# Kernel tuning notes

Measured on AMD Instinct MI355X. Metric: run time of the kernel, lower is better.

The kernel has to match this reference:

```python
import jax, jax.numpy as jnp
import numpy as np

T, H, NH, HD, I = 2048, 2048, 16, 128, 8192
EPS = 1e-6


def rotate_every_two(x):
    # result[..., 2i] = -x[..., 2i+1]; result[..., 2i+1] = x[..., 2i]
    x1 = x[..., ::2]
    x2 = x[..., 1::2]
    return jnp.stack((-x2, x1), axis=-1).reshape(x.shape)


def setup_inputs() -> dict:
    key = jax.random.key(0)
    ks = jax.random.split(key, 10)
    x = jax.random.normal(ks[0], (T, H), dtype=jnp.float32)
    normed_ages = jax.random.normal(ks[1], (T,), dtype=jnp.float32)
    sin = jax.random.uniform(ks[2], (T, 1, HD), dtype=jnp.float32)
    cos = jax.random.uniform(ks[3], (T, 1, HD), dtype=jnp.float32)
    attn_bias = jax.random.normal(ks[4], (1, NH, T, T), dtype=jnp.float32) * 0.02
    norm_w = jnp.ones((H,), dtype=jnp.float32)
    w_in = jax.random.normal(ks[5], (H, 3 * H + 2 * I), dtype=jnp.float32) / np.sqrt(H)
    b_in = jnp.zeros((3 * H + 2 * I,), dtype=jnp.float32)
    w_out = jax.random.normal(ks[6], (H + I, H), dtype=jnp.float32) / np.sqrt(H + I)
    b_out = jnp.zeros((H,), dtype=jnp.float32)
    return {"x": x, "normed_ages": normed_ages, "sin": sin, "cos": cos,
            "attn_bias": attn_bias, "norm_w": norm_w, "w_in": w_in,
            "b_in": b_in, "w_out": w_out, "b_out": b_out}


def reference(x, normed_ages, sin, cos, attn_bias, norm_w, b_in, b_out, w_in, w_out):
    # RMSNorm
    xn = x * jax.lax.rsqrt(jnp.mean(x * x, axis=-1, keepdims=True) + EPS) * norm_w
    # use_normed_ages: overwrite last two feature columns
    xn = xn.at[:, -2].set(normed_ages)
    xn = xn.at[:, -1].set(normed_ages * normed_ages)
    # fused input projection: [T, 2I (ff) | 3H (qkv)]
    t = xn @ w_in + b_in
    ff = t[:, : 2 * I]
    qkv = t[:, 2 * I:].reshape(T, 3, NH, HD)
    q = qkv[:, 0] * cos + rotate_every_two(qkv[:, 0]) * sin  # [T, NH, HD]
    k = qkv[:, 1] * cos + rotate_every_two(qkv[:, 1]) * sin
    v = qkv[:, 2]
    # attention (xformers memory_efficient_attention semantics, scale 1/sqrt(HD))
    scores = jnp.einsum('thd,shd->hts', q, k) / np.sqrt(HD) + attn_bias[0]
    probs = jax.nn.softmax(scores, axis=-1)
    attn = jnp.einsum('hts,shd->thd', probs, v).reshape(T, H)
    # SwiGLU
    x1, x2 = ff[:, :I], ff[:, I:]
    ff = jax.nn.silu(x1) * x2
    combined = jnp.concatenate((attn, ff), axis=-1)  # [T, H+I]
    return combined @ w_out + b_out
```

## Files before the change

kernel.cpp:

```cpp
#include <hip/hip_runtime.h>
#include <stdint.h>

typedef unsigned short u16;
typedef __attribute__((ext_vector_type(8))) short short8;
typedef __attribute__((ext_vector_type(4))) short short4v;
typedef __attribute__((ext_vector_type(4))) float floatx4;

#define T_DIM 2048
#define NH    16
#define HD    128
#define H_DIM 2048
#define I_DIM 8192
#define NCOL1 22528
#define NCOL2 10240
#define PADW  1036
#define KSPLIT 4
#define KSLEN  (NCOL2 / KSPLIT)

__device__ __forceinline__ float bf2f(u16 b) {
  union { uint32_t u; float f; } x; x.u = ((uint32_t)b) << 16; return x.f;
}
__device__ __forceinline__ u16 f2bf(float f) {
  union { float f; uint32_t u; } x; x.f = f;
  uint32_t r = x.u + 0x7fffu + ((x.u >> 16) & 1u);
  return (u16)(r >> 16);
}

__device__ __forceinline__ void gl_lds16(const void* g, void* l) {
  __builtin_amdgcn_global_load_lds((const __attribute__((address_space(1))) void*)g,
                                   (__attribute__((address_space(3))) void*)l, 16, 0, 0);
}

__device__ __forceinline__ floatx4 mfma32(short8 a, short8 b, floatx4 c) {
  return __builtin_amdgcn_mfma_f32_16x16x32_bf16(a, b, c, 0, 0, 0);
}
__device__ __forceinline__ floatx4 mfma16(short4v a, short4v b, floatx4 c) {
#if __has_builtin(__builtin_amdgcn_mfma_f32_16x16x16bf16_1k)
  return __builtin_amdgcn_mfma_f32_16x16x16bf16_1k(a, b, c, 0, 0, 0);
#else
  asm volatile("v_mfma_f32_16x16x16_bf16 %0, %1, %2, %0" : "+v"(c) : "v"(a), "v"(b));
  return c;
#endif
}

__global__ __launch_bounds__(256) void rmsnorm_k(
    const float* __restrict__ x, const float* __restrict__ ages,
    const float* __restrict__ w, u16* __restrict__ xn) {
  int t = blockIdx.x, tid = threadIdx.x;
  const float* xr = x + (size_t)t * H_DIM;
  floatx4 a = *(const floatx4*)(xr + tid * 8);
  floatx4 b = *(const floatx4*)(xr + tid * 8 + 4);
  float ss = a[0]*a[0]+a[1]*a[1]+a[2]*a[2]+a[3]*a[3]
           + b[0]*b[0]+b[1]*b[1]+b[2]*b[2]+b[3]*b[3];
#pragma unroll
  for (int off = 32; off >= 1; off >>= 1) ss += __shfl_xor(ss, off);
  __shared__ float red[4];
  if ((tid & 63) == 0) red[tid >> 6] = ss;
  __syncthreads();
  float tot = red[0] + red[1] + red[2] + red[3];
  float rms = rsqrtf(tot * (1.0f / H_DIM) + 1e-6f);
  const float* wr = w + tid * 8;
  float v[8] = {a[0],a[1],a[2],a[3],b[0],b[1],b[2],b[3]};
  short8 o;
#pragma unroll
  for (int i = 0; i < 8; ++i) o[i] = (short)f2bf(v[i] * rms * wr[i]);
  if (tid == 255) {
    float ag = ages[t];
    o[6] = (short)f2bf(ag);
    o[7] = (short)f2bf(ag * ag);
  }
  *(short8*)(xn + (size_t)t * H_DIM + tid * 8) = o;
}

__global__ __launch_bounds__(256) void transpose_f32_bf16(
    const float* __restrict__ in, u16* __restrict__ out, int K, int N) {
  __shared__ float tile[32][33];
  int n0 = blockIdx.x * 32, k0 = blockIdx.y * 32;
  int c = threadIdx.x & 31, r = threadIdx.x >> 5;
#pragma unroll
  for (int i = 0; i < 4; ++i) {
    int kk = r + i * 8;
    tile[c][kk] = in[(size_t)(k0 + kk) * N + n0 + c];
  }
  __syncthreads();
#pragma unroll
  for (int i = 0; i < 4; ++i) {
    int nn = r + i * 8;
    out[(size_t)(n0 + nn) * K + k0 + c] = f2bf(tile[nn][c]);
  }
}

template<int OUTF>
__global__ __launch_bounds__(256, 2) void gemm_bt(
    const u16* __restrict__ A, const u16* __restrict__ B,
    const float* __restrict__ bias, void* __restrict__ Cout,
    int M, int N, int K, int klen) {
  __shared__ __align__(16) u16 sm[32768];
  int nbm = M >> 7, nbn = N >> 7;
  int per = nbm * nbn;
  int nwg = per * (K / klen);
  int bid = blockIdx.x;
  int swz = (bid & 7) * (nwg >> 3) + (bid >> 3);
  int sp = swz / per, rr = swz % per;
  int bn = rr / nbm, bm = rr % nbm;
  int kbeg = sp * klen;
  int tid = threadIdx.x, lane = tid & 63, w = tid >> 6;
  int wr = tid >> 7, wc = (tid >> 6) & 1;
  int lq = lane & 15, lg = lane >> 4;

  int srow = lane >> 2;
  int scol = (((lane & 3) ^ ((lane >> 3) & 3)) << 3);
  const u16* Ag0 = A + (size_t)(bm * 128 + w * 32 + srow) * K + kbeg + scol;
  const u16* Ag1 = Ag0 + (size_t)16 * K;
  const u16* Bg0 = B + (size_t)(bn * 128 + w * 32 + srow) * K + kbeg + scol;
  const u16* Bg1 = Bg0 + (size_t)16 * K;
  u16* Ad0 = sm + w * 1024 + lane * 8;
  u16* Ad1 = Ad0 + 512;
  u16* Bd0 = sm + 4096 + w * 1024 + lane * 8;
  u16* Bd1 = Bd0 + 512;

  int xorc = ((lq >> 1) & 3) << 3;
  int aoff = (wr * 64 + lq) * 32 + ((lg * 8) ^ xorc);
  int boff = 4096 + (wc * 64 + lq) * 32 + ((lg * 8) ^ xorc);

  floatx4 acc[4][4] = {};
  const int NT = klen >> 5;

  auto STAGE = [&](int t) {
    int sl = (t & 3) * 8192;
    int ko = t * 32;
    gl_lds16(Ag0 + ko, Ad0 + sl);
    gl_lds16(Ag1 + ko, Ad1 + sl);
    gl_lds16(Bg0 + ko, Bd0 + sl);
    gl_lds16(Bg1 + ko, Bd1 + sl);
  };

  STAGE(0); STAGE(1); STAGE(2);
  asm volatile("s_waitcnt vmcnt(8)\n\ts_barrier" ::: "memory");

  for (int t = 0; t < NT; ++t) {
    if (t + 3 < NT) STAGE(t + 3);
    const u16* sb = sm + (t & 3) * 8192;
    short8 af[4], bf[4];
#pragma unroll
    for (int i = 0; i < 4; ++i) af[i] = *(const short8*)(sb + aoff + i * 512);
#pragma unroll
    for (int i = 0; i < 4; ++i) bf[i] = *(const short8*)(sb + boff + i * 512);
    __builtin_amdgcn_s_setprio(1);
#pragma unroll
    for (int mi = 0; mi < 4; ++mi)
#pragma unroll
      for (int ni = 0; ni < 4; ++ni)
        acc[mi][ni] = mfma32(af[mi], bf[ni], acc[mi][ni]);
    __builtin_amdgcn_s_setprio(0);
    if (t + 3 < NT) asm volatile("s_waitcnt vmcnt(8)\n\ts_barrier" ::: "memory");
    else            asm volatile("s_waitcnt vmcnt(0)\n\ts_barrier" ::: "memory");
  }

#pragma unroll
  for (int mi = 0; mi < 4; ++mi) {
#pragma unroll
    for (int ni = 0; ni < 4; ++ni) {
      int col = bn * 128 + wc * 64 + ni * 16 + lq;
      float bv = (OUTF == 2) ? 0.f : bias[col];
#pragma unroll
      for (int j = 0; j < 4; ++j) {
        int row = bm * 128 + wr * 64 + mi * 16 + lg * 4 + j;
        float vv = acc[mi][ni][j] + bv;
        if (OUTF == 0)      ((u16*)Cout)[(size_t)row * N + col] = f2bf(vv);
        else if (OUTF == 1) ((float*)Cout)[(size_t)row * N + col] = vv;
        else ((float*)Cout)[(size_t)sp * M * N + (size_t)row * N + col] = vv;
      }
    }
  }
}

__global__ __launch_bounds__(256) void reduce_split(
    const float* __restrict__ part, const float* __restrict__ bias,
    float* __restrict__ out) {
  size_t idx = ((size_t)blockIdx.x * 256 + threadIdx.x) * 4;
  int col = (int)(idx & (H_DIM - 1));
  floatx4 acc = *(const floatx4*)(bias + col);
#pragma unroll
  for (int s = 0; s < KSPLIT; ++s) {
    floatx4 p = *(const floatx4*)(part + (size_t)s * T_DIM * H_DIM + idx);
#pragma unroll
    for (int j = 0; j < 4; ++j) acc[j] += p[j];
  }
  *(floatx4*)(out + idx) = acc;
}

__global__ __launch_bounds__(256) void rope_split(
    const u16* __restrict__ tb, const float* __restrict__ sinp, const float* __restrict__ cosp,
    u16* __restrict__ qb, u16* __restrict__ kf, u16* __restrict__ vf) {
  __shared__ u16 vtile[32][130];
  int t0 = blockIdx.x * 32, h = blockIdx.y, tid = threadIdx.x;
  int r = tid >> 3, d0 = (tid & 7) << 4;
  int t = t0 + r;
  const u16* base = tb + (size_t)t * NCOL1 + 2 * I_DIM + h * HD + d0;
  const float* cp = cosp + (size_t)t * HD + d0;
  const float* sp = sinp + (size_t)t * HD + d0;
  float cv[16], sv[16];
#pragma unroll
  for (int i = 0; i < 16; i += 4) {
    *(floatx4*)(cv + i) = *(const floatx4*)(cp + i);
    *(floatx4*)(sv + i) = *(const floatx4*)(sp + i);
  }
#pragma unroll
  for (int s = 0; s < 2; ++s) {
    const u16* src = base + s * (NH * HD);
    short8 x0 = *(const short8*)src;
    short8 x1 = *(const short8*)(src + 8);
    float xf[16];
#pragma unroll
    for (int i = 0; i < 8; ++i) { xf[i] = bf2f((u16)x0[i]); xf[8 + i] = bf2f((u16)x1[i]); }
    short8 o0, o1;
#pragma unroll
    for (int i = 0; i < 8; i += 2) {
      o0[i]     = (short)f2bf(xf[i] * cv[i] - xf[i + 1] * sv[i]);
      o0[i + 1] = (short)f2bf(xf[i + 1] * cv[i + 1] + xf[i] * sv[i + 1]);
      o1[i]     = (short)f2bf(xf[8 + i] * cv[8 + i] - xf[9 + i] * sv[8 + i]);
      o1[i + 1] = (short)f2bf(xf[9 + i] * cv[9 + i] + xf[8 + i] * sv[9 + i]);
    }
    if (s == 0) {
      u16* dst = qb + ((size_t)h * T_DIM + t) * HD + d0;
      *(short8*)dst = o0;
      *(short8*)(dst + 8) = o1;
    } else {
      int s16 = t >> 4, tt = d0 >> 5, lg0 = (d0 >> 3) & 3;
      size_t cb = (((size_t)h * 128 + s16) * 4 + tt) * 512 + ((t & 15) + 16 * lg0) * 8;
      *(short8*)(kf + cb) = o0;
      *(short8*)(kf + cb + 128) = o1;
    }
  }
  short8 v0 = *(const short8*)(base + 2 * NH * HD);
  short8 v1 = *(const short8*)(base + 2 * NH * HD + 8);
#pragma unroll
  for (int i = 0; i < 8; ++i) {
    vtile[r][d0 + i]     = (u16)v0[i];
    vtile[r][d0 + 8 + i] = (u16)v1[i];
  }
  __syncthreads();
  {
    int d = tid >> 1, th = (tid & 1) << 4;
    int s16 = (t0 + th) >> 4;
    int dp = d >> 5, par = (d >> 4) & 1, lqv = d & 15;
    size_t cb = (((size_t)h * 128 + s16) * 4 + dp) * 512 + par * 4;
#pragma unroll
    for (int lg = 0; lg < 4; ++lg) {
      short4v g;
#pragma unroll
      for (int j = 0; j < 4; ++j) g[j] = (short)vtile[th + lg * 4 + j][d];
      *(short4v*)(vf + cb + (size_t)(lqv + 16 * lg) * 8) = g;
    }
  }
}

__global__ __launch_bounds__(256) void silu_mul(
    const u16* __restrict__ tb, u16* __restrict__ comb) {
  int idx = blockIdx.x * 256 + threadIdx.x;
  int t = idx >> 10;
  int j = (idx & 1023) << 3;
  const u16* p1 = tb + (size_t)t * NCOL1 + j;
  const u16* p2 = p1 + I_DIM;
  short8 a = *(const short8*)p1;
  short8 b = *(const short8*)p2;
  short8 o;
#pragma unroll
  for (int i = 0; i < 8; ++i) {
    float x1 = bf2f((u16)a[i]), x2 = bf2f((u16)b[i]);
    float s = x1 / (1.0f + __expf(-x1));
    o[i] = (short)f2bf(s * x2);
  }
  *(short8*)(comb + (size_t)t * NCOL2 + H_DIM + j) = o;
}

__global__ __launch_bounds__(256) void attn_fused(
    const u16* __restrict__ Q, const u16* __restrict__ kf,
    const u16* __restrict__ vf, const float* __restrict__ bias,
    u16* __restrict__ comb) {
  __shared__ float lds[16 * PADW];
  int bid = blockIdx.x;
  int swz = (bid & 7) * 256 + (bid >> 3);
  int h = swz >> 7, qt = swz & 127;
  int q0 = qt * 16;
  int tid = threadIdx.x;
  int w = tid >> 6, lane = tid & 63;
  int lq = lane & 15, lg = lane >> 4;

  const u16* Qp = Q + ((size_t)h * T_DIM + q0 + lq) * HD + lg * 8;
  const u16* Kf = kf + ((size_t)h * 128) * 2048 + lane * 8;
  const u16* Vf = vf + ((size_t)h * 128) * 2048 + lane * 8;
  const float* Bh = bias + ((size_t)h * T_DIM + q0) * T_DIM;

  short8 qf[4];
#pragma unroll
  for (int t = 0; t < 4; ++t) qf[t] = *(const short8*)(Qp + t * 32);

  floatx4 o[8] = {};
  float m = -1e30f, l = 0.f;
  const float sc = 0.08838834764831845f;

#pragma unroll
  for (int tile = 0; tile < 2; ++tile) {
#pragma unroll
    for (int r = 0; r < 16; ++r) {
      const float* src = Bh + (size_t)r * T_DIM + tile * 1024 + tid * 4;
      gl_lds16(src, &lds[r * PADW + tid * 4]);
    }
    __syncthreads();
#pragma unroll
    for (int sub = 0; sub < 8; ++sub) {
      int soff = sub * 128 + w * 32;
      int s0 = tile * 1024 + soff;
      int s16a = s0 >> 4;
      const u16* ka = Kf + (size_t)s16a * 2048;
      floatx4 st0 = {0.f,0.f,0.f,0.f}, st1 = {0.f,0.f,0.f,0.f};
#pragma unroll
      for (int t = 0; t < 4; ++t) {
        st0 = mfma32(*(const short8*)(ka + t * 512), qf[t], st0);
        st1 = mfma32(*(const short8*)(ka + 2048 + t * 512), qf[t], st1);
      }
      floatx4 b0 = *(const floatx4*)&lds[lq * PADW + soff + lg * 4];
      floatx4 b1 = *(const floatx4*)&lds[lq * PADW + soff + lg * 4 + 16];
      float p[8]; float tmax = -1e30f;
#pragma unroll
      for (int j = 0; j < 4; ++j) {
        p[j]     = st0[j] * sc + b0[j];
        p[4 + j] = st1[j] * sc + b1[j];
        tmax = fmaxf(tmax, fmaxf(p[j], p[4 + j]));
      }
      tmax = fmaxf(tmax, __shfl_xor(tmax, 16));
      tmax = fmaxf(tmax, __shfl_xor(tmax, 32));
      float mn = fmaxf(m, tmax);
      float alpha = __expf(m - mn);
      float rs = 0.f;
      short4v pb0, pb1;
#pragma unroll
      for (int j = 0; j < 4; ++j) {
        float e0 = __expf(p[j] - mn), e1 = __expf(p[4 + j] - mn);
        rs += e0 + e1;
        pb0[j] = (short)f2bf(e0);
        pb1[j] = (short)f2bf(e1);
      }
      rs += __shfl_xor(rs, 16);
      rs += __shfl_xor(rs, 32);
      l = l * alpha + rs; m = mn;
#pragma unroll
      for (int dt = 0; dt < 8; ++dt) o[dt] *= alpha;
      const u16* vb = Vf + (size_t)s16a * 2048;
#pragma unroll
      for (int dp = 0; dp < 4; ++dp) {
        short8 wa = *(const short8*)(vb + dp * 512);
        short8 wb = *(const short8*)(vb + 2048 + dp * 512);
        short4v a0 = {wa[0], wa[1], wa[2], wa[3]};
        short4v a1 = {wa[4], wa[5], wa[6], wa[7]};
        short4v c0 = {wb[0], wb[1], wb[2], wb[3]};
        short4v c1 = {wb[4], wb[5], wb[6], wb[7]};
        o[2*dp]     = mfma16(a0, pb0, o[2*dp]);
        o[2*dp + 1] = mfma16(a1, pb0, o[2*dp + 1]);
        o[2*dp]     = mfma16(c0, pb1, o[2*dp]);
        o[2*dp + 1] = mfma16(c1, pb1, o[2*dp + 1]);
      }
    }
    __syncthreads();
  }

  if (lg == 0) { lds[8448 + w * 16 + lq] = m; lds[8512 + w * 16 + lq] = l; }
  __syncthreads();
  float M = -1e30f;
#pragma unroll
  for (int i = 0; i < 4; ++i) M = fmaxf(M, lds[8448 + i * 16 + lq]);
  float scale = __expf(m - M);
#pragma unroll
  for (int dt = 0; dt < 8; ++dt) {
    floatx4 so = o[dt] * scale;
    *(floatx4*)&lds[w * 2112 + lq * 132 + dt * 16 + lg * 4] = so;
  }
  __syncthreads();
  {
    int row = tid >> 4, d0 = (tid & 15) * 8;
    float M2 = -1e30f;
#pragma unroll
    for (int i = 0; i < 4; ++i) M2 = fmaxf(M2, lds[8448 + i * 16 + row]);
    float den = 0.f;
#pragma unroll
    for (int i = 0; i < 4; ++i)
      den += __expf(lds[8448 + i * 16 + row] - M2) * lds[8512 + i * 16 + row];
    float inv = 1.0f / den;
    short8 ov;
#pragma unroll
    for (int k = 0; k < 8; ++k) {
      float s = 0.f;
#pragma unroll
      for (int i = 0; i < 4; ++i) s += lds[i * 2112 + row * 132 + d0 + k];
      ov[k] = (short)f2bf(s * inv);
    }
    *(short8*)(comb + (size_t)(q0 + row) * NCOL2 + h * HD + d0) = ov;
  }
}

extern "C" void kernel_launch(void* const* d_in, const int* in_sizes, int n_in,
                              void* d_out, int out_size, void* d_ws, size_t ws_size,
                              hipStream_t stream) {
  (void)in_sizes; (void)n_in; (void)out_size; (void)ws_size;
  const float* x     = (const float*)d_in[0];
  const float* ages  = (const float*)d_in[1];
  const float* sinp  = (const float*)d_in[2];
  const float* cosp  = (const float*)d_in[3];
  const float* bias  = (const float*)d_in[4];
  const float* normw = (const float*)d_in[5];
  const float* w_in  = (const float*)d_in[6];
  const float* b_in  = (const float*)d_in[7];
  const float* w_out = (const float*)d_in[8];
  const float* b_out = (const float*)d_in[9];

  char* ws = (char*)d_ws;
  const size_t SZ_XN   = (size_t)T_DIM * H_DIM * 2;
  const size_t SZ_W1T  = (size_t)NCOL1 * H_DIM * 2;
  const size_t SZ_T    = (size_t)T_DIM * NCOL1 * 2;
  const size_t SZ_HEAD = (size_t)NH * T_DIM * HD * 2;
  u16* xn   = (u16*)(ws);
  u16* w1t  = (u16*)(ws + SZ_XN);
  u16* tb   = (u16*)(ws + SZ_XN + SZ_W1T);
  u16* qb   = (u16*)(ws + SZ_XN + SZ_W1T + SZ_T);
  u16* kf   = (u16*)(ws + SZ_XN + SZ_W1T + SZ_T + SZ_HEAD);
  u16* vf   = (u16*)(ws + SZ_XN + SZ_W1T + SZ_T + 2 * SZ_HEAD);
  u16* w2t  = (u16*)(ws + SZ_XN);
  u16* comb = (u16*)(ws + SZ_XN + (48ull << 20));
  float* part = (float*)tb;

  rmsnorm_k<<<T_DIM, 256, 0, stream>>>(x, ages, normw, xn);
  transpose_f32_bf16<<<dim3(NCOL1 / 32, H_DIM / 32), 256, 0, stream>>>(w_in, w1t, H_DIM, NCOL1);
  gemm_bt<0><<<(T_DIM / 128) * (NCOL1 / 128), 256, 0, stream>>>(
      xn, w1t, b_in, tb, T_DIM, NCOL1, H_DIM, H_DIM);
  rope_split<<<dim3(T_DIM / 32, NH), 256, 0, stream>>>(tb, sinp, cosp, qb, kf, vf);
  silu_mul<<<(T_DIM * I_DIM) / (256 * 8), 256, 0, stream>>>(tb, comb);
  transpose_f32_bf16<<<dim3(H_DIM / 32, NCOL2 / 32), 256, 0, stream>>>(w_out, w2t, NCOL2, H_DIM);
  attn_fused<<<NH * (T_DIM / 16), 256, 0, stream>>>(qb, kf, vf, bias, comb);
  gemm_bt<2><<<(T_DIM / 128) * (H_DIM / 128) * KSPLIT, 256, 0, stream>>>(
      comb, w2t, b_out, part, T_DIM, H_DIM, NCOL2, KSLEN);
  reduce_split<<<(T_DIM * H_DIM / 4) / 256, 256, 0, stream>>>(part, b_out, (float*)d_out);
}
```

Measured before the change: 612.3 us.

## Enlarge GEMM tiles to 256x256 with 512-thread workgroups

```diff
diff --git a/kernel.cpp b/kernel.cpp
--- a/kernel.cpp
+++ b/kernel.cpp
@@ -91,12 +91,12 @@
 }
 
 template<int OUTF>
-__global__ __launch_bounds__(256, 2) void gemm_bt(
+__global__ __launch_bounds__(512, 2) void gemm256(
     const u16* __restrict__ A, const u16* __restrict__ B,
     const float* __restrict__ bias, void* __restrict__ Cout,
     int M, int N, int K, int klen) {
-  __shared__ __align__(16) u16 sm[32768];
-  int nbm = M >> 7, nbn = N >> 7;
+  __shared__ __align__(16) u16 sm[65536];
+  int nbm = M >> 8, nbn = N >> 8;
   int per = nbm * nbn;
   int nwg = per * (K / klen);
   int bid = blockIdx.x;
@@ -104,30 +104,32 @@
   int sp = swz / per, rr = swz % per;
   int bn = rr / nbm, bm = rr % nbm;
   int kbeg = sp * klen;
-  int tid = threadIdx.x, lane = tid & 63, w = tid >> 6;
-  int wr = tid >> 7, wc = (tid >> 6) & 1;
+  int tid = threadIdx.x, lane = tid & 63;
+  int wid = tid >> 6;
+  int wrow = wid >> 2;
+  int wcol = wid & 3;
   int lq = lane & 15, lg = lane >> 4;
 
-  int srow = lane >> 2;
-  int scol = (((lane & 3) ^ ((lane >> 3) & 3)) << 3);
-  const u16* Ag0 = A + (size_t)(bm * 128 + w * 32 + srow) * K + kbeg + scol;
-  const u16* Ag1 = Ag0 + (size_t)16 * K;
-  const u16* Bg0 = B + (size_t)(bn * 128 + w * 32 + srow) * K + kbeg + scol;
-  const u16* Bg1 = Bg0 + (size_t)16 * K;
-  u16* Ad0 = sm + w * 1024 + lane * 8;
-  u16* Ad1 = Ad0 + 512;
-  u16* Bd0 = sm + 4096 + w * 1024 + lane * 8;
-  u16* Bd1 = Bd0 + 512;
+  int srow = tid >> 2;
+  int scol = ((tid & 3) ^ ((tid >> 3) & 3)) << 3;
+  const u16* Ag0 = A + (size_t)(bm * 256 + srow) * K + kbeg + scol;
+  const u16* Ag1 = Ag0 + (size_t)128 * K;
+  const u16* Bg0 = B + (size_t)(bn * 256 + srow) * K + kbeg + scol;
+  const u16* Bg1 = Bg0 + (size_t)128 * K;
+  u16* Ad0 = sm + tid * 8;
+  u16* Ad1 = sm + 4096 + tid * 8;
+  u16* Bd0 = sm + 8192 + tid * 8;
+  u16* Bd1 = sm + 12288 + tid * 8;
 
   int xorc = ((lq >> 1) & 3) << 3;
-  int aoff = (wr * 64 + lq) * 32 + ((lg * 8) ^ xorc);
-  int boff = 4096 + (wc * 64 + lq) * 32 + ((lg * 8) ^ xorc);
-
-  floatx4 acc[4][4] = {};
+  int aoff = (wrow * 128 + lq) * 32 + ((lg * 8) ^ xorc);
+  int boff = 8192 + (wcol * 64 + lq) * 32 + ((lg * 8) ^ xorc);
+
+  floatx4 acc[8][4] = {};
   const int NT = klen >> 5;
 
   auto STAGE = [&](int t) {
-    int sl = (t & 3) * 8192;
+    int sl = (t & 3) * 16384;
     int ko = t * 32;
     gl_lds16(Ag0 + ko, Ad0 + sl);
     gl_lds16(Ag1 + ko, Ad1 + sl);
@@ -140,32 +142,32 @@
 
   for (int t = 0; t < NT; ++t) {
     if (t + 3 < NT) STAGE(t + 3);
-    const u16* sb = sm + (t & 3) * 8192;
-    short8 af[4], bf[4];
-#pragma unroll
-    for (int i = 0; i < 4; ++i) af[i] = *(const short8*)(sb + aoff + i * 512);
-#pragma unroll
-    for (int i = 0; i < 4; ++i) bf[i] = *(const short8*)(sb + boff + i * 512);
+    const u16* sb = sm + (t & 3) * 16384;
+    short8 af[8], bfr[4];
+#pragma unroll
+    for (int i = 0; i < 8; ++i) af[i]  = *(const short8*)(sb + aoff + i * 512);
+#pragma unroll
+    for (int i = 0; i < 4; ++i) bfr[i] = *(const short8*)(sb + boff + i * 512);
     __builtin_amdgcn_s_setprio(1);
 #pragma unroll
-    for (int mi = 0; mi < 4; ++mi)
+    for (int mi = 0; mi < 8; ++mi)
 #pragma unroll
       for (int ni = 0; ni < 4; ++ni)
-        acc[mi][ni] = mfma32(af[mi], bf[ni], acc[mi][ni]);
+        acc[mi][ni] = mfma32(af[mi], bfr[ni], acc[mi][ni]);
     __builtin_amdgcn_s_setprio(0);
     if (t + 3 < NT) asm volatile("s_waitcnt vmcnt(8)\n\ts_barrier" ::: "memory");
     else            asm volatile("s_waitcnt vmcnt(0)\n\ts_barrier" ::: "memory");
   }
 
 #pragma unroll
-  for (int mi = 0; mi < 4; ++mi) {
+  for (int mi = 0; mi < 8; ++mi) {
 #pragma unroll
     for (int ni = 0; ni < 4; ++ni) {
-      int col = bn * 128 + wc * 64 + ni * 16 + lq;
+      int col = bn * 256 + wcol * 64 + ni * 16 + lq;
       float bv = (OUTF == 2) ? 0.f : bias[col];
 #pragma unroll
       for (int j = 0; j < 4; ++j) {
-        int row = bm * 128 + wr * 64 + mi * 16 + lg * 4 + j;
+        int row = bm * 256 + wrow * 128 + mi * 16 + lg * 4 + j;
         float vv = acc[mi][ni][j] + bv;
         if (OUTF == 0)      ((u16*)Cout)[(size_t)row * N + col] = f2bf(vv);
         else if (OUTF == 1) ((float*)Cout)[(size_t)row * N + col] = vv;
@@ -432,13 +434,13 @@
 
   rmsnorm_k<<<T_DIM, 256, 0, stream>>>(x, ages, normw, xn);
   transpose_f32_bf16<<<dim3(NCOL1 / 32, H_DIM / 32), 256, 0, stream>>>(w_in, w1t, H_DIM, NCOL1);
-  gemm_bt<0><<<(T_DIM / 128) * (NCOL1 / 128), 256, 0, stream>>>(
+  gemm256<0><<<(T_DIM / 256) * (NCOL1 / 256), 512, 0, stream>>>(
       xn, w1t, b_in, tb, T_DIM, NCOL1, H_DIM, H_DIM);
   rope_split<<<dim3(T_DIM / 32, NH), 256, 0, stream>>>(tb, sinp, cosp, qb, kf, vf);
   silu_mul<<<(T_DIM * I_DIM) / (256 * 8), 256, 0, stream>>>(tb, comb);
   transpose_f32_bf16<<<dim3(H_DIM / 32, NCOL2 / 32), 256, 0, stream>>>(w_out, w2t, NCOL2, H_DIM);
   attn_fused<<<NH * (T_DIM / 16), 256, 0, stream>>>(qb, kf, vf, bias, comb);
-  gemm_bt<2><<<(T_DIM / 128) * (H_DIM / 128) * KSPLIT, 256, 0, stream>>>(
+  gemm256<2><<<(T_DIM / 256) * (H_DIM / 256) * KSPLIT, 512, 0, stream>>>(
       comb, w2t, b_out, part, T_DIM, H_DIM, NCOL2, KSLEN);
   reduce_split<<<(T_DIM * H_DIM / 4) / 256, 256, 0, stream>>>(part, b_out, (float*)d_out);
 }
```

After: 548.3 us. 1.12x faster.
